# Performance work log

Hardware: AMD Instinct MI355X
Metric: run time of the kernel (lower is better)

## Reference

```python
import jax, jax.numpy as jnp
import numpy as np

G, B, S, D = 4, 1, 1024, 2048   # num_gpus (chunks), batch, seq_local, model dim
H, DH = 32, 64                  # heads, dim_head; inner_dim = H*DH = D
EPS = 1e-6
NEG = -1e30                     # finite stand-in for -inf lse init (grad-safe)


def setup_inputs() -> dict:
    key = jax.random.key(0)
    ks = jax.random.split(key, 8)
    wsc = 1.0 / np.sqrt(D)  # keep pre-softmax logits in a sane range
    return {
        'x':  jax.random.normal(ks[0], (G, B, S, D), jnp.float32),
        'Wq': jax.random.normal(ks[1], (D, D), jnp.float32) * wsc,
        'bq': jnp.zeros((D,), jnp.float32),
        'Wk': jax.random.normal(ks[2], (D, D), jnp.float32) * wsc,
        'bk': jnp.zeros((D,), jnp.float32),
        'Wv': jax.random.normal(ks[3], (D, D), jnp.float32) * wsc,
        'bv': jnp.zeros((D,), jnp.float32),
        'qn_w': jnp.ones((D,), jnp.float32),
        'kn_w': jnp.ones((D,), jnp.float32),
        'Wo': jax.random.normal(ks[4], (D, D), jnp.float32) * wsc,
        'bo': jnp.zeros((D,), jnp.float32),
    }


def _rms_norm(t, w):
    return t * jax.lax.rsqrt(jnp.mean(t * t, axis=-1, keepdims=True) + EPS) * w


def reference(x, Wq, bq, Wk, bk, Wv, bv, qn_w, kn_w, Wo, bo):
    # x: [G, B, S, D] -- per-'GPU' sequence chunks
    q = _rms_norm(x @ Wq.T + bq, qn_w)
    k = _rms_norm(x @ Wk.T + bk, kn_w)
    v = x @ Wv.T + bv
    split = lambda t: t.reshape(G, B, S, H, DH).transpose(0, 1, 3, 2, 4)  # [G,B,H,S,DH]
    q, k, v = split(q), split(k), split(v)
    scale = 1.0 / np.sqrt(DH)

    out = jnp.zeros_like(q)
    lse = jnp.full((G, B, H, S, 1), NEG, q.dtype)
    kc, vc = k, v
    # Ring: each chunk attends to the visiting K/V chunk with online softmax.
    for _ in range(G):
        scores = jnp.einsum('gbhqd,gbhkd->gbhqk', q, kc) * scale
        m = scores.max(axis=-1, keepdims=True)
        e = jnp.exp(scores - m)
        ssum = e.sum(axis=-1, keepdims=True)
        chunk_lse = m + jnp.log(ssum)
        chunk_out = jnp.einsum('gbhqk,gbhkd->gbhqd', e / ssum, vc)
        new_lse = jnp.logaddexp(lse, chunk_lse)
        out = out * jnp.exp(lse - new_lse) + chunk_out * jnp.exp(chunk_lse - new_lse)
        lse = new_lse
        # rotate K/V around the ring: device i receives from device i-1
        kc = jnp.roll(kc, 1, axis=0)
        vc = jnp.roll(vc, 1, axis=0)

    o = out.transpose(0, 1, 3, 2, 4).reshape(G, B, S, H * DH)
    return o @ Wo.T + bo
```

## Files before the change

kernel.cpp:

```cpp
#include <hip/hip_runtime.h>

typedef __bf16 bf16x8 __attribute__((ext_vector_type(8)));
typedef float f32x4 __attribute__((ext_vector_type(4)));
typedef float f32x16 __attribute__((ext_vector_type(16)));
typedef unsigned short u16x8 __attribute__((ext_vector_type(8)));
typedef unsigned u32x2 __attribute__((ext_vector_type(2)));
typedef unsigned u32x4 __attribute__((ext_vector_type(4)));

__device__ __forceinline__ unsigned short f2bf(float f) {
  union { float f; unsigned u; } v; v.f = f;
  unsigned r = (v.u + 0x7fffu + ((v.u >> 16) & 1u)) >> 16;
  return (unsigned short)r;
}
__device__ __forceinline__ float bf2f(unsigned short s) {
  union { unsigned u; float f; } v; v.u = ((unsigned)s) << 16;
  return v.f;
}

#define GLD16(g, l)                                                        \
  __builtin_amdgcn_global_load_lds(                                        \
      (const __attribute__((address_space(1))) void*)(g),                  \
      (__attribute__((address_space(3))) void*)(l), 16, 0, 0)

__device__ __forceinline__ int swzc(int row, int colel) {
  return colel ^ ((((row & 7) ^ ((row >> 3) & 7)) & 7) << 3);
}

__device__ __forceinline__ u32x2 plswap(unsigned a, unsigned b) {
  return __builtin_amdgcn_permlane32_swap(a, b, false, false);
}
__device__ __forceinline__ float pair_sum(float x) {
  u32x2 r = plswap(__float_as_uint(x), __float_as_uint(x));
  return __uint_as_float(r.x) + __uint_as_float(r.y);
}
__device__ __forceinline__ unsigned cvtpk(float a, float b) {
  unsigned r;
  asm("v_cvt_pk_bf16_f32 %0, %1, %2" : "=v"(r) : "v"(a), "v"(b));
  return r;
}

__global__ __launch_bounds__(256) void cast_bf16_kernel(
    const float* __restrict__ in, unsigned short* __restrict__ out, int n4) {
  int i = blockIdx.x * 256 + threadIdx.x;
  int stride = gridDim.x * 256;
  for (; i < n4; i += stride) {
    float4 f = reinterpret_cast<const float4*>(in)[i];
    ushort4 s;
    s.x = f2bf(f.x); s.y = f2bf(f.y); s.z = f2bf(f.z); s.w = f2bf(f.w);
    reinterpret_cast<ushort4*>(out)[i] = s;
  }
}

__global__ __launch_bounds__(256) void cast_w4_kernel(
    const float* __restrict__ w0, const float* __restrict__ w1,
    const float* __restrict__ w2, const float* __restrict__ w3,
    unsigned short* __restrict__ o0, unsigned short* __restrict__ o1,
    unsigned short* __restrict__ o2, unsigned short* __restrict__ o3) {
  int i = blockIdx.x * 256 + threadIdx.x;
  int stride = gridDim.x * 256;
  for (; i < 4194304; i += stride) {
    int sel = i >> 20;
    const float* src = sel == 0 ? w0 : sel == 1 ? w1 : sel == 2 ? w2 : w3;
    unsigned short* dst = sel == 0 ? o0 : sel == 1 ? o1 : sel == 2 ? o2 : o3;
    int j = i & 1048575;
    float4 f = reinterpret_cast<const float4*>(src)[j];
    ushort4 s;
    s.x = f2bf(f.x); s.y = f2bf(f.y); s.z = f2bf(f.z); s.w = f2bf(f.w);
    reinterpret_cast<ushort4*>(dst)[j] = s;
  }
}

#define STG_A(STEP, KS, BUF)                                                   \
  GLD16(Ag + (size_t)(row0 + st_row0) * 2048 + (STEP) * 64 + (KS) * 32 +       \
            st_col0,                                                           \
        &ls[((BUF) * 2 + (KS)) * 4096 + (wid * 2) * 512]);                     \
  GLD16(Ag + (size_t)(row0 + st_row1) * 2048 + (STEP) * 64 + (KS) * 32 +       \
            st_col1,                                                           \
        &ls[((BUF) * 2 + (KS)) * 4096 + (wid * 2 + 1) * 512]);

#define STG_B(STEP, KS, BUF)                                                   \
  GLD16(Bg + (size_t)(col0 + st_row0) * 2048 + (STEP) * 64 + (KS) * 32 +       \
            st_col0,                                                           \
        &ls[16384 + ((BUF) * 2 + (KS)) * 4096 + (wid * 2) * 512]);             \
  GLD16(Bg + (size_t)(col0 + st_row1) * 2048 + (STEP) * 64 + (KS) * 32 +       \
            st_col1,                                                           \
        &ls[16384 + ((BUF) * 2 + (KS)) * 4096 + (wid * 2 + 1) * 512]);

#define VM8 asm volatile("s_waitcnt vmcnt(8)" ::: "memory");
#define VM4 asm volatile("s_waitcnt vmcnt(4)" ::: "memory");
#define VM0 asm volatile("s_waitcnt vmcnt(0)" ::: "memory");

#define PHASE(BUF, KS, MQ, RB, STG, VMW)                                       \
  {                                                                            \
    af0 = *(const bf16x8*)&ls[((BUF) * 2 + (KS)) * 4096 + offA[(MQ) * 2 + 0]]; \
    af1 = *(const bf16x8*)&ls[((BUF) * 2 + (KS)) * 4096 + offA[(MQ) * 2 + 1]]; \
    if (RB) {                                                                  \
      bfr[0] = *(const bf16x8*)&ls[16384 + ((BUF) * 2 + (KS)) * 4096 + offB[0]]; \
      bfr[1] = *(const bf16x8*)&ls[16384 + ((BUF) * 2 + (KS)) * 4096 + offB[1]]; \
      bfr[2] = *(const bf16x8*)&ls[16384 + ((BUF) * 2 + (KS)) * 4096 + offB[2]]; \
      bfr[3] = *(const bf16x8*)&ls[16384 + ((BUF) * 2 + (KS)) * 4096 + offB[3]]; \
    }                                                                          \
    STG;                                                                       \
    __builtin_amdgcn_s_barrier();                                              \
    __builtin_amdgcn_s_setprio(1);                                             \
    acc[(MQ) * 2 + 0][0] = __builtin_amdgcn_mfma_f32_16x16x32_bf16(            \
        af0, bfr[0], acc[(MQ) * 2 + 0][0], 0, 0, 0);                           \
    acc[(MQ) * 2 + 0][1] = __builtin_amdgcn_mfma_f32_16x16x32_bf16(            \
        af0, bfr[1], acc[(MQ) * 2 + 0][1], 0, 0, 0);                           \
    acc[(MQ) * 2 + 0][2] = __builtin_amdgcn_mfma_f32_16x16x32_bf16(            \
        af0, bfr[2], acc[(MQ) * 2 + 0][2], 0, 0, 0);                           \
    acc[(MQ) * 2 + 0][3] = __builtin_amdgcn_mfma_f32_16x16x32_bf16(            \
        af0, bfr[3], acc[(MQ) * 2 + 0][3], 0, 0, 0);                           \
    acc[(MQ) * 2 + 1][0] = __builtin_amdgcn_mfma_f32_16x16x32_bf16(            \
        af1, bfr[0], acc[(MQ) * 2 + 1][0], 0, 0, 0);                           \
    acc[(MQ) * 2 + 1][1] = __builtin_amdgcn_mfma_f32_16x16x32_bf16(            \
        af1, bfr[1], acc[(MQ) * 2 + 1][1], 0, 0, 0);                           \
    acc[(MQ) * 2 + 1][2] = __builtin_amdgcn_mfma_f32_16x16x32_bf16(            \
        af1, bfr[2], acc[(MQ) * 2 + 1][2], 0, 0, 0);                           \
    acc[(MQ) * 2 + 1][3] = __builtin_amdgcn_mfma_f32_16x16x32_bf16(            \
        af1, bfr[3], acc[(MQ) * 2 + 1][3], 0, 0, 0);                           \
    __builtin_amdgcn_s_setprio(0);                                             \
    VMW;                                                                       \
    __builtin_amdgcn_s_barrier();                                              \
  }

template <int F32OUT>
__global__ __launch_bounds__(256, 2) void gemm8p(
    const unsigned short* __restrict__ Ag,
    const unsigned short* __restrict__ W0, const unsigned short* __restrict__ W1,
    const unsigned short* __restrict__ W2,
    const float* __restrict__ b0, const float* __restrict__ b1,
    const float* __restrict__ b2,
    void* __restrict__ C0, void* __restrict__ C1, void* __restrict__ C2) {
  extern __shared__ __align__(16) unsigned short ls[];

  const int lin = blockIdx.y * gridDim.x + blockIdx.x;
  const int cpx = (gridDim.x * gridDim.y) >> 3;
  const int swz = (lin & 7) * cpx + (lin >> 3);
  const int bx = swz % gridDim.x, by = swz / gridDim.x;

  const int gcol = bx * 128;
  const int sel = gcol >> 11;
  const unsigned short* Bg = sel == 0 ? W0 : sel == 1 ? W1 : W2;
  const float* bias = sel == 0 ? b0 : sel == 1 ? b1 : b2;
  void* Cp = sel == 0 ? C0 : sel == 1 ? C1 : C2;
  const int col0 = gcol & 2047;
  const int row0 = by * 128;

  const int tid = threadIdx.x, lane = tid & 63, wid = tid >> 6;
  const int l15 = lane & 15, l4 = lane >> 4;
  const int wm = wid >> 1, wn = wid & 1;

  const int ci0 = wid * 2, ci1 = wid * 2 + 1;
  const int st_row0 = ci0 * 16 + (lane >> 2);
  const int st_row1 = ci1 * 16 + (lane >> 2);
  const int sl2a = ((lane >> 2) & 3) ^ ((lane >> 4) & 3);
  const int st_col0 = (((lane & 3) ^ (sl2a ^ (ci0 & 3))) * 8);
  const int st_col1 = (((lane & 3) ^ (sl2a ^ (ci1 & 3))) * 8);

  const int lsel = (l15 & 3) ^ ((l15 >> 2) & 3);
  int offA[4], offB[4];
#pragma unroll
  for (int f = 0; f < 4; ++f)
    offA[f] = (wm * 64 + f * 16 + l15) * 32 + ((l4 ^ lsel ^ (f & 3)) & 3) * 8;
#pragma unroll
  for (int ni = 0; ni < 4; ++ni)
    offB[ni] =
        (wn * 64 + ni * 16 + l15) * 32 + ((l4 ^ lsel ^ ((wn * 4 + ni) & 3)) & 3) * 8;

  f32x4 acc[4][4] = {};
  bf16x8 af0, af1, bfr[4];

  STG_A(0, 0, 0); STG_B(0, 0, 0);
  STG_A(0, 1, 0); STG_B(0, 1, 0);
  STG_A(1, 0, 1); STG_B(1, 0, 1);
  VM8;
  __builtin_amdgcn_s_barrier();

  for (int it = 0; it < 15; ++it) {
    const int sE = 2 * it, sO = sE + 1;
    PHASE(0, 0, 0, 1, STG_A(sO, 1, 1), );
    PHASE(0, 0, 1, 0, STG_B(sO, 1, 1), VM8);
    PHASE(0, 1, 0, 1, STG_A(sE + 2, 0, 0), );
    PHASE(0, 1, 1, 0, STG_B(sE + 2, 0, 0), VM8);
    PHASE(1, 0, 0, 1, STG_A(sE + 2, 1, 0), );
    PHASE(1, 0, 1, 0, STG_B(sE + 2, 1, 0), VM8);
    PHASE(1, 1, 0, 1, STG_A(sO + 2, 0, 1), );
    PHASE(1, 1, 1, 0, STG_B(sO + 2, 0, 1), VM8);
  }
  PHASE(0, 0, 0, 1, STG_A(31, 1, 1), );
  PHASE(0, 0, 1, 0, STG_B(31, 1, 1), VM8);
  PHASE(0, 1, 0, 1, , );
  PHASE(0, 1, 1, 0, , VM4);
  PHASE(1, 0, 0, 1, , );
  PHASE(1, 0, 1, 0, , VM0);
  PHASE(1, 1, 0, 1, , );
  PHASE(1, 1, 1, 0, , );

#pragma unroll
  for (int f = 0; f < 4; ++f)
#pragma unroll
    for (int ni = 0; ni < 4; ++ni)
#pragma unroll
      for (int r = 0; r < 4; ++r) {
        int row = row0 + wm * 64 + f * 16 + l4 * 4 + r;
        int col = col0 + wn * 64 + ni * 16 + l15;
        float v = acc[f][ni][r] + bias[col];
        if (F32OUT)
          ((float*)Cp)[(size_t)row * 2048 + col] = v;
        else
          ((unsigned short*)Cp)[(size_t)row * 2048 + col] = f2bf(v);
      }
}

__global__ __launch_bounds__(256) void rmsnorm2_kernel(
    unsigned short* __restrict__ Qb, unsigned short* __restrict__ Kb,
    const float* __restrict__ qw, const float* __restrict__ kw) {
  const int row = blockIdx.x;
  unsigned short* p;
  const float* w;
  if (row < 4096) { p = Qb + (size_t)row * 2048; w = qw; }
  else            { p = Kb + (size_t)(row - 4096) * 2048; w = kw; }
  const int tid = threadIdx.x;
  u16x8 v = *(const u16x8*)&p[tid * 8];
  float f[8];
  float ss = 0.f;
#pragma unroll
  for (int j = 0; j < 8; ++j) { f[j] = bf2f(v[j]); ss += f[j] * f[j]; }
#pragma unroll
  for (int m = 1; m < 64; m <<= 1) ss += __shfl_xor(ss, m, 64);
  __shared__ float red[4];
  const int wid = tid >> 6, lane = tid & 63;
  if (lane == 0) red[wid] = ss;
  __syncthreads();
  float tot = red[0] + red[1] + red[2] + red[3];
  float rs = rsqrtf(tot * (1.0f / 2048.0f) + 1e-6f);
  u16x8 o;
#pragma unroll
  for (int j = 0; j < 8; ++j) o[j] = f2bf(f[j] * rs * w[tid * 8 + j]);
  *(u16x8*)&p[tid * 8] = o;
}

__global__ __launch_bounds__(256, 2) void flash_attn(
    const unsigned short* __restrict__ Q, const unsigned short* __restrict__ K,
    const unsigned short* __restrict__ V, unsigned short* __restrict__ O) {
  __shared__ unsigned short Ks[2][64 * 64];
  __shared__ unsigned short Vs[2][64 * 64];
  const int bid = blockIdx.x;
  const int sw = (bid & 7) * 64 + (bid >> 3);
  const int h = sw >> 4;
  const int q0 = (sw & 15) * 256;
  const int tid = threadIdx.x, lane = tid & 63, wid = tid >> 6;
  const int l31 = lane & 31, hi = lane >> 5;

  const int kr0 = wid * 16 + (lane >> 3);
  const int kc0 = (lane & 7) * 8;
  const int vkey = (tid & 31) * 2;
  const int vd0 = (tid >> 5) * 8;

  const float QSCALE = 0.125f * 1.44269504f;
  bf16x8 qf0[4], qf1[4];
  {
    const int qr0 = q0 + wid * 64 + l31;
#pragma unroll
    for (int kt = 0; kt < 4; ++kt) {
      bf16x8 r0 = *(const bf16x8*)&Q[(size_t)qr0 * 2048 + h * 64 + kt * 16 + hi * 8];
      bf16x8 r1 = *(const bf16x8*)&Q[(size_t)(qr0 + 32) * 2048 + h * 64 + kt * 16 + hi * 8];
#pragma unroll
      for (int j = 0; j < 8; ++j) {
        qf0[kt][j] = (__bf16)((float)r0[j] * QSCALE);
        qf1[kt][j] = (__bf16)((float)r1[j] * QSCALE);
      }
    }
  }

  int off[2][4];
#pragma unroll
  for (int kb = 0; kb < 2; ++kb) {
    const int row = kb * 32 + l31;
    const int sl = (((row & 7) ^ ((row >> 3) & 7)) & 7) << 3;
#pragma unroll
    for (int kt = 0; kt < 4; ++kt)
      off[kb][kt] = row * 64 + ((kt * 16 + hi * 8) ^ sl);
  }

  float l0 = 0.f, l1 = 0.f;
  f32x16 oa0[2] = {}, oa1[2] = {};

  u16x8 kreg0, kreg1, vreg0, vreg1;
  auto loadKV = [&](int kt0) {
    kreg0 = *(const u16x8*)&K[(size_t)(kt0 + kr0) * 2048 + h * 64 + kc0];
    kreg1 = *(const u16x8*)&K[(size_t)(kt0 + kr0 + 8) * 2048 + h * 64 + kc0];
    vreg0 = *(const u16x8*)&V[(size_t)(kt0 + vkey) * 2048 + h * 64 + vd0];
    vreg1 = *(const u16x8*)&V[(size_t)(kt0 + vkey + 1) * 2048 + h * 64 + vd0];
  };
  auto writeKV = [&](int b) {
    *(u16x8*)&Ks[b][kr0 * 64 + swzc(kr0, kc0)] = kreg0;
    *(u16x8*)&Ks[b][(kr0 + 8) * 64 + swzc(kr0 + 8, kc0)] = kreg1;
#pragma unroll
    for (int d = 0; d < 8; ++d) {
      int row = vd0 + d;
      *(unsigned*)&Vs[b][row * 64 + swzc(row, vkey)] =
          (unsigned)vreg0[d] | ((unsigned)vreg1[d] << 16);
    }
  };

  loadKV(0);
  writeKV(0);
  __syncthreads();

  for (int t = 0; t < 64; ++t) {
    const int cur = t & 1;
    if (t < 63) loadKV((t + 1) * 64);

    const unsigned short* Kc = Ks[cur];
    const unsigned short* Vc = Vs[cur];

    bf16x8 kf[2][4];
#pragma unroll
    for (int kb = 0; kb < 2; ++kb)
#pragma unroll
      for (int kt = 0; kt < 4; ++kt)
        kf[kb][kt] = *(const bf16x8*)&Kc[off[kb][kt]];

    f32x16 st0[2], st1[2];
    __builtin_amdgcn_s_setprio(1);
#pragma unroll
    for (int kb = 0; kb < 2; ++kb) {
      f32x16 a = {};
#pragma unroll
      for (int kt = 0; kt < 4; ++kt)
        a = __builtin_amdgcn_mfma_f32_32x32x16_bf16(kf[kb][kt], qf0[kt], a, 0, 0, 0);
      st0[kb] = a;
    }
#pragma unroll
    for (int kb = 0; kb < 2; ++kb) {
      f32x16 a = {};
#pragma unroll
      for (int kt = 0; kt < 4; ++kt)
        a = __builtin_amdgcn_mfma_f32_32x32x16_bf16(kf[kb][kt], qf1[kt], a, 0, 0, 0);
      st1[kb] = a;
    }
    __builtin_amdgcn_s_setprio(0);

    unsigned pk0[16], pk1[16];
    {
      float s0 = 0.f, s1 = 0.f, s2 = 0.f, s3 = 0.f;
#pragma unroll
      for (int kb = 0; kb < 2; ++kb)
#pragma unroll
        for (int j = 0; j < 8; ++j) {
          float pa = __builtin_amdgcn_exp2f(st0[kb][2 * j]);
          float pb = __builtin_amdgcn_exp2f(st0[kb][2 * j + 1]);
          if ((j & 3) == 0) s0 += pa + pb;
          else if ((j & 3) == 1) s1 += pa + pb;
          else if ((j & 3) == 2) s2 += pa + pb;
          else s3 += pa + pb;
          pk0[kb * 8 + j] = cvtpk(pa, pb);
        }
      l0 += (s0 + s1) + (s2 + s3);
    }
    {
      float s0 = 0.f, s1 = 0.f, s2 = 0.f, s3 = 0.f;
#pragma unroll
      for (int kb = 0; kb < 2; ++kb)
#pragma unroll
        for (int j = 0; j < 8; ++j) {
          float pa = __builtin_amdgcn_exp2f(st1[kb][2 * j]);
          float pb = __builtin_amdgcn_exp2f(st1[kb][2 * j + 1]);
          if ((j & 3) == 0) s0 += pa + pb;
          else if ((j & 3) == 1) s1 += pa + pb;
          else if ((j & 3) == 2) s2 += pa + pb;
          else s3 += pa + pb;
          pk1[kb * 8 + j] = cvtpk(pa, pb);
        }
      l1 += (s0 + s1) + (s2 + s3);
    }

    bf16x8 pfrag0[4], pfrag1[4];
#pragma unroll
    for (int kt = 0; kt < 4; ++kt) {
      u32x2 sa = plswap(pk0[4 * kt + 0], pk0[4 * kt + 2]);
      u32x2 sb = plswap(pk0[4 * kt + 1], pk0[4 * kt + 3]);
      union { u32x4 u; bf16x8 b; } w;
      w.u.x = sa.x; w.u.y = sb.x; w.u.z = sa.y; w.u.w = sb.y;
      pfrag0[kt] = w.b;
      u32x2 sc = plswap(pk1[4 * kt + 0], pk1[4 * kt + 2]);
      u32x2 sd = plswap(pk1[4 * kt + 1], pk1[4 * kt + 3]);
      union { u32x4 u; bf16x8 b; } w2;
      w2.u.x = sc.x; w2.u.y = sd.x; w2.u.z = sc.y; w2.u.w = sd.y;
      pfrag1[kt] = w2.b;
    }

    __builtin_amdgcn_s_setprio(1);
#pragma unroll
    for (int dv = 0; dv < 2; ++dv) {
      bf16x8 vf[4];
#pragma unroll
      for (int kt = 0; kt < 4; ++kt)
        vf[kt] = *(const bf16x8*)&Vc[off[dv][kt]];
#pragma unroll
      for (int kt = 0; kt < 4; ++kt)
        oa0[dv] = __builtin_amdgcn_mfma_f32_32x32x16_bf16(vf[kt], pfrag0[kt], oa0[dv], 0, 0, 0);
#pragma unroll
      for (int kt = 0; kt < 4; ++kt)
        oa1[dv] = __builtin_amdgcn_mfma_f32_32x32x16_bf16(vf[kt], pfrag1[kt], oa1[dv], 0, 0, 0);
    }
    __builtin_amdgcn_s_setprio(0);

    if (t < 63) {
      writeKV(cur ^ 1);
      __syncthreads();
    }
  }

  const float inv0 = 1.0f / pair_sum(l0);
  const float inv1 = 1.0f / pair_sum(l1);
  const int qr0 = q0 + wid * 64 + l31;
#pragma unroll
  for (int dv = 0; dv < 2; ++dv)
#pragma unroll
    for (int tq = 0; tq < 4; ++tq) {
      int dh = 32 * dv + 8 * tq + 4 * hi;
      unsigned a0 = cvtpk(oa0[dv][4 * tq + 0] * inv0, oa0[dv][4 * tq + 1] * inv0);
      unsigned a1 = cvtpk(oa0[dv][4 * tq + 2] * inv0, oa0[dv][4 * tq + 3] * inv0);
      u32x2 wa = {a0, a1};
      *(u32x2*)&O[(size_t)qr0 * 2048 + h * 64 + dh] = wa;
      unsigned b0 = cvtpk(oa1[dv][4 * tq + 0] * inv1, oa1[dv][4 * tq + 1] * inv1);
      unsigned b1 = cvtpk(oa1[dv][4 * tq + 2] * inv1, oa1[dv][4 * tq + 3] * inv1);
      u32x2 wb = {b0, b1};
      *(u32x2*)&O[(size_t)(qr0 + 32) * 2048 + h * 64 + dh] = wb;
    }
}

extern "C" void kernel_launch(void* const* d_in, const int* in_sizes, int n_in,
                              void* d_out, int out_size, void* d_ws, size_t ws_size,
                              hipStream_t stream) {
  const float* x  = (const float*)d_in[0];
  const float* Wq = (const float*)d_in[1];
  const float* bq = (const float*)d_in[2];
  const float* Wk = (const float*)d_in[3];
  const float* bk = (const float*)d_in[4];
  const float* Wv = (const float*)d_in[5];
  const float* bv = (const float*)d_in[6];
  const float* qn = (const float*)d_in[7];
  const float* kn = (const float*)d_in[8];
  const float* Wo = (const float*)d_in[9];
  const float* bo = (const float*)d_in[10];

  char* w = (char*)d_ws;
  unsigned short* Xbf = (unsigned short*)(w);
  unsigned short* Wqb = (unsigned short*)(w + 16777216);
  unsigned short* Wkb = (unsigned short*)(w + 25165824);
  unsigned short* Wvb = (unsigned short*)(w + 33554432);
  unsigned short* Wob = (unsigned short*)(w + 41943040);
  unsigned short* Qb  = (unsigned short*)(w + 50331648);
  unsigned short* Kb  = (unsigned short*)(w + 67108864);
  unsigned short* Vb  = (unsigned short*)(w + 83886080);
  unsigned short* Ob  = Xbf;

  cast_bf16_kernel<<<1024, 256, 0, stream>>>(x, Xbf, 8388608 / 4);
  cast_w4_kernel<<<2048, 256, 0, stream>>>(Wq, Wk, Wv, Wo, Wqb, Wkb, Wvb, Wob);

  gemm8p<0><<<dim3(48, 32), 256, 65536, stream>>>(
      Xbf, Wqb, Wkb, Wvb, bq, bk, bv, Qb, Kb, Vb);

  rmsnorm2_kernel<<<8192, 256, 0, stream>>>(Qb, Kb, qn, kn);

  flash_attn<<<512, 256, 0, stream>>>(Qb, Kb, Vb, Ob);

  gemm8p<1><<<dim3(16, 32), 256, 65536, stream>>>(
      Ob, Wob, Wob, Wob, bo, bo, bo, d_out, d_out, d_out);
}
```

Before: 359.8 us.

## Merge GEMM half-phases into four full phases and fuse cast kernels

The GEMM main loop is restructured from eight half-phases per iteration, each doing 8 MFMAs, to four phases per iteration. Each phase loads all A and B fragments, issues both A and B global-to-LDS stages, and runs 16 MFMAs. This halves the number of barriers and waitcnt points per K-step, at the cost of higher register pressure and coarser interleaving of loads with compute. Separately, the input cast and the weight cast are merged into one kernel launch to save launch overhead.

```diff
diff --git a/kernel.cpp b/kernel.cpp
--- a/kernel.cpp
+++ b/kernel.cpp
@@ -39,36 +39,35 @@
   return r;
 }
 
-__global__ __launch_bounds__(256) void cast_bf16_kernel(
-    const float* __restrict__ in, unsigned short* __restrict__ out, int n4) {
-  int i = blockIdx.x * 256 + threadIdx.x;
-  int stride = gridDim.x * 256;
-  for (; i < n4; i += stride) {
-    float4 f = reinterpret_cast<const float4*>(in)[i];
-    ushort4 s;
-    s.x = f2bf(f.x); s.y = f2bf(f.y); s.z = f2bf(f.z); s.w = f2bf(f.w);
-    reinterpret_cast<ushort4*>(out)[i] = s;
-  }
-}
-
-__global__ __launch_bounds__(256) void cast_w4_kernel(
+__global__ __launch_bounds__(256) void cast_all_kernel(
+    const float* __restrict__ x,
     const float* __restrict__ w0, const float* __restrict__ w1,
     const float* __restrict__ w2, const float* __restrict__ w3,
+    unsigned short* __restrict__ xo,
     unsigned short* __restrict__ o0, unsigned short* __restrict__ o1,
     unsigned short* __restrict__ o2, unsigned short* __restrict__ o3) {
   int i = blockIdx.x * 256 + threadIdx.x;
   int stride = gridDim.x * 256;
-  for (; i < 4194304; i += stride) {
-    int sel = i >> 20;
-    const float* src = sel == 0 ? w0 : sel == 1 ? w1 : sel == 2 ? w2 : w3;
-    unsigned short* dst = sel == 0 ? o0 : sel == 1 ? o1 : sel == 2 ? o2 : o3;
-    int j = i & 1048575;
+  for (; i < 6291456; i += stride) {
+    const float* src;
+    unsigned short* dst;
+    int j;
+    if (i < 2097152) {
+      src = x; dst = xo; j = i;
+    } else {
+      int k = i - 2097152;
+      int sel = k >> 20;
+      src = sel == 0 ? w0 : sel == 1 ? w1 : sel == 2 ? w2 : w3;
+      dst = sel == 0 ? o0 : sel == 1 ? o1 : sel == 2 ? o2 : o3;
+      j = k & 1048575;
+    }
     float4 f = reinterpret_cast<const float4*>(src)[j];
     ushort4 s;
     s.x = f2bf(f.x); s.y = f2bf(f.y); s.z = f2bf(f.z); s.w = f2bf(f.w);
     reinterpret_cast<ushort4*>(dst)[j] = s;
   }
 }
+
 
 #define STG_A(STEP, KS, BUF)                                                   \
   GLD16(Ag + (size_t)(row0 + st_row0) * 2048 + (STEP) * 64 + (KS) * 32 +       \
@@ -90,42 +89,43 @@
 #define VM4 asm volatile("s_waitcnt vmcnt(4)" ::: "memory");
 #define VM0 asm volatile("s_waitcnt vmcnt(0)" ::: "memory");
 
-#define PHASE(BUF, KS, MQ, RB, STG, VMW)                                       \
+#define PHASE4(BUF, KS, STG, VMW)                                              \
   {                                                                            \
-    af0 = *(const bf16x8*)&ls[((BUF) * 2 + (KS)) * 4096 + offA[(MQ) * 2 + 0]]; \
-    af1 = *(const bf16x8*)&ls[((BUF) * 2 + (KS)) * 4096 + offA[(MQ) * 2 + 1]]; \
-    if (RB) {                                                                  \
-      bfr[0] = *(const bf16x8*)&ls[16384 + ((BUF) * 2 + (KS)) * 4096 + offB[0]]; \
-      bfr[1] = *(const bf16x8*)&ls[16384 + ((BUF) * 2 + (KS)) * 4096 + offB[1]]; \
-      bfr[2] = *(const bf16x8*)&ls[16384 + ((BUF) * 2 + (KS)) * 4096 + offB[2]]; \
-      bfr[3] = *(const bf16x8*)&ls[16384 + ((BUF) * 2 + (KS)) * 4096 + offB[3]]; \
-    }                                                                          \
+    const int pb = ((BUF) * 2 + (KS)) * 4096;                                  \
+    bf16x8 af0 = *(const bf16x8*)&ls[pb + offA[0]];                            \
+    bf16x8 af1 = *(const bf16x8*)&ls[pb + offA[1]];                            \
+    bf16x8 af2 = *(const bf16x8*)&ls[pb + offA[2]];                            \
+    bf16x8 af3 = *(const bf16x8*)&ls[pb + offA[3]];                            \
+    bf16x8 bf0 = *(const bf16x8*)&ls[16384 + pb + offB[0]];                    \
+    bf16x8 bf1 = *(const bf16x8*)&ls[16384 + pb + offB[1]];                    \
+    bf16x8 bf2 = *(const bf16x8*)&ls[16384 + pb + offB[2]];                    \
+    bf16x8 bf3 = *(const bf16x8*)&ls[16384 + pb + offB[3]];                    \
     STG;                                                                       \
     __builtin_amdgcn_s_barrier();                                              \
     __builtin_amdgcn_s_setprio(1);                                             \
-    acc[(MQ) * 2 + 0][0] = __builtin_amdgcn_mfma_f32_16x16x32_bf16(            \
-        af0, bfr[0], acc[(MQ) * 2 + 0][0], 0, 0, 0);                           \
-    acc[(MQ) * 2 + 0][1] = __builtin_amdgcn_mfma_f32_16x16x32_bf16(            \
-        af0, bfr[1], acc[(MQ) * 2 + 0][1], 0, 0, 0);                           \
-    acc[(MQ) * 2 + 0][2] = __builtin_amdgcn_mfma_f32_16x16x32_bf16(            \
-        af0, bfr[2], acc[(MQ) * 2 + 0][2], 0, 0, 0);                           \
-    acc[(MQ) * 2 + 0][3] = __builtin_amdgcn_mfma_f32_16x16x32_bf16(            \
-        af0, bfr[3], acc[(MQ) * 2 + 0][3], 0, 0, 0);                           \
-    acc[(MQ) * 2 + 1][0] = __builtin_amdgcn_mfma_f32_16x16x32_bf16(            \
-        af1, bfr[0], acc[(MQ) * 2 + 1][0], 0, 0, 0);                           \
-    acc[(MQ) * 2 + 1][1] = __builtin_amdgcn_mfma_f32_16x16x32_bf16(            \
-        af1, bfr[1], acc[(MQ) * 2 + 1][1], 0, 0, 0);                           \
-    acc[(MQ) * 2 + 1][2] = __builtin_amdgcn_mfma_f32_16x16x32_bf16(            \
-        af1, bfr[2], acc[(MQ) * 2 + 1][2], 0, 0, 0);                           \
-    acc[(MQ) * 2 + 1][3] = __builtin_amdgcn_mfma_f32_16x16x32_bf16(            \
-        af1, bfr[3], acc[(MQ) * 2 + 1][3], 0, 0, 0);                           \
+    acc[0][0] = __builtin_amdgcn_mfma_f32_16x16x32_bf16(af0, bf0, acc[0][0], 0, 0, 0); \
+    acc[0][1] = __builtin_amdgcn_mfma_f32_16x16x32_bf16(af0, bf1, acc[0][1], 0, 0, 0); \
+    acc[0][2] = __builtin_amdgcn_mfma_f32_16x16x32_bf16(af0, bf2, acc[0][2], 0, 0, 0); \
+    acc[0][3] = __builtin_amdgcn_mfma_f32_16x16x32_bf16(af0, bf3, acc[0][3], 0, 0, 0); \
+    acc[1][0] = __builtin_amdgcn_mfma_f32_16x16x32_bf16(af1, bf0, acc[1][0], 0, 0, 0); \
+    acc[1][1] = __builtin_amdgcn_mfma_f32_16x16x32_bf16(af1, bf1, acc[1][1], 0, 0, 0); \
+    acc[1][2] = __builtin_amdgcn_mfma_f32_16x16x32_bf16(af1, bf2, acc[1][2], 0, 0, 0); \
+    acc[1][3] = __builtin_amdgcn_mfma_f32_16x16x32_bf16(af1, bf3, acc[1][3], 0, 0, 0); \
+    acc[2][0] = __builtin_amdgcn_mfma_f32_16x16x32_bf16(af2, bf0, acc[2][0], 0, 0, 0); \
+    acc[2][1] = __builtin_amdgcn_mfma_f32_16x16x32_bf16(af2, bf1, acc[2][1], 0, 0, 0); \
+    acc[2][2] = __builtin_amdgcn_mfma_f32_16x16x32_bf16(af2, bf2, acc[2][2], 0, 0, 0); \
+    acc[2][3] = __builtin_amdgcn_mfma_f32_16x16x32_bf16(af2, bf3, acc[2][3], 0, 0, 0); \
+    acc[3][0] = __builtin_amdgcn_mfma_f32_16x16x32_bf16(af3, bf0, acc[3][0], 0, 0, 0); \
+    acc[3][1] = __builtin_amdgcn_mfma_f32_16x16x32_bf16(af3, bf1, acc[3][1], 0, 0, 0); \
+    acc[3][2] = __builtin_amdgcn_mfma_f32_16x16x32_bf16(af3, bf2, acc[3][2], 0, 0, 0); \
+    acc[3][3] = __builtin_amdgcn_mfma_f32_16x16x32_bf16(af3, bf3, acc[3][3], 0, 0, 0); \
     __builtin_amdgcn_s_setprio(0);                                             \
     VMW;                                                                       \
     __builtin_amdgcn_s_barrier();                                              \
   }
 
 template <int F32OUT>
-__global__ __launch_bounds__(256, 2) void gemm8p(
+__global__ __launch_bounds__(256, 2) void gemm4p(
     const unsigned short* __restrict__ Ag,
     const unsigned short* __restrict__ W0, const unsigned short* __restrict__ W1,
     const unsigned short* __restrict__ W2,
@@ -169,7 +169,6 @@
         (wn * 64 + ni * 16 + l15) * 32 + ((l4 ^ lsel ^ ((wn * 4 + ni) & 3)) & 3) * 8;
 
   f32x4 acc[4][4] = {};
-  bf16x8 af0, af1, bfr[4];
 
   STG_A(0, 0, 0); STG_B(0, 0, 0);
   STG_A(0, 1, 0); STG_B(0, 1, 0);
@@ -179,23 +178,15 @@
 
   for (int it = 0; it < 15; ++it) {
     const int sE = 2 * it, sO = sE + 1;
-    PHASE(0, 0, 0, 1, STG_A(sO, 1, 1), );
-    PHASE(0, 0, 1, 0, STG_B(sO, 1, 1), VM8);
-    PHASE(0, 1, 0, 1, STG_A(sE + 2, 0, 0), );
-    PHASE(0, 1, 1, 0, STG_B(sE + 2, 0, 0), VM8);
-    PHASE(1, 0, 0, 1, STG_A(sE + 2, 1, 0), );
-    PHASE(1, 0, 1, 0, STG_B(sE + 2, 1, 0), VM8);
-    PHASE(1, 1, 0, 1, STG_A(sO + 2, 0, 1), );
-    PHASE(1, 1, 1, 0, STG_B(sO + 2, 0, 1), VM8);
-  }
-  PHASE(0, 0, 0, 1, STG_A(31, 1, 1), );
-  PHASE(0, 0, 1, 0, STG_B(31, 1, 1), VM8);
-  PHASE(0, 1, 0, 1, , );
-  PHASE(0, 1, 1, 0, , VM4);
-  PHASE(1, 0, 0, 1, , );
-  PHASE(1, 0, 1, 0, , VM0);
-  PHASE(1, 1, 0, 1, , );
-  PHASE(1, 1, 1, 0, , );
+    PHASE4(0, 0, STG_A(sO, 1, 1) STG_B(sO, 1, 1), VM8);
+    PHASE4(0, 1, STG_A(sE + 2, 0, 0) STG_B(sE + 2, 0, 0), VM8);
+    PHASE4(1, 0, STG_A(sE + 2, 1, 0) STG_B(sE + 2, 1, 0), VM8);
+    PHASE4(1, 1, STG_A(sO + 2, 0, 1) STG_B(sO + 2, 0, 1), VM8);
+  }
+  PHASE4(0, 0, STG_A(31, 1, 1) STG_B(31, 1, 1), VM8);
+  PHASE4(0, 1, , VM4);
+  PHASE4(1, 0, , VM0);
+  PHASE4(1, 1, , );
 
 #pragma unroll
   for (int f = 0; f < 4; ++f)
@@ -459,16 +450,16 @@
   unsigned short* Vb  = (unsigned short*)(w + 83886080);
   unsigned short* Ob  = Xbf;
 
-  cast_bf16_kernel<<<1024, 256, 0, stream>>>(x, Xbf, 8388608 / 4);
-  cast_w4_kernel<<<2048, 256, 0, stream>>>(Wq, Wk, Wv, Wo, Wqb, Wkb, Wvb, Wob);
-
-  gemm8p<0><<<dim3(48, 32), 256, 65536, stream>>>(
+  cast_all_kernel<<<3072, 256, 0, stream>>>(x, Wq, Wk, Wv, Wo,
+                                            Xbf, Wqb, Wkb, Wvb, Wob);
+
+  gemm4p<0><<<dim3(48, 32), 256, 65536, stream>>>(
       Xbf, Wqb, Wkb, Wvb, bq, bk, bv, Qb, Kb, Vb);
 
   rmsnorm2_kernel<<<8192, 256, 0, stream>>>(Qb, Kb, qn, kn);
 
   flash_attn<<<512, 256, 0, stream>>>(Qb, Kb, Vb, Ob);
 
-  gemm8p<1><<<dim3(16, 32), 256, 65536, stream>>>(
+  gemm4p<1><<<dim3(16, 32), 256, 65536, stream>>>(
       Ob, Wob, Wob, Wob, bo, bo, bo, d_out, d_out, d_out);
 }
```

After: 362.4 us. No clear change (+0.7%).
